# Performance work log

Measured on AMD Instinct MI355X. Metric: run time of the kernel, lower is better.

## Reference

```python
import jax, jax.numpy as jnp
import numpy as np

D = 1024
B, N = 4, 2048

def setup_inputs() -> dict:
    key = jax.random.key(0)
    ks = jax.random.split(key, 7)
    sc = 1.0 / np.sqrt(D)
    return {
        "x": jax.random.normal(ks[0], (B, N, D), dtype=jnp.float32),
        "wq_w": jax.random.normal(ks[1], (D, D), dtype=jnp.float32) * sc,
        "wq_b": jax.random.normal(ks[2], (D,), dtype=jnp.float32) * 0.01,
        "wk_w": jax.random.normal(ks[3], (D, D), dtype=jnp.float32) * sc,
        "wk_b": jax.random.normal(ks[4], (D,), dtype=jnp.float32) * 0.01,
        "wv_w": jax.random.normal(ks[5], (D, D), dtype=jnp.float32) * sc,
        "wv_b": jax.random.normal(ks[6], (D,), dtype=jnp.float32) * 0.01,
    }

def reference(x, wq_w, wq_b, wk_w, wk_b, wv_w, wv_b):
    # torch Linear: y = x @ W^T + b
    q = x @ wq_w.T + wq_b
    k = x @ wk_w.T + wk_b
    v = x @ wv_w.T + wv_b
    d = q.shape[-1]
    s = jnp.einsum("bid,bjd->bij", q, k) / jnp.sqrt(jnp.float32(d))
    # faithful to original: triu then transpose (zeros, NOT -inf, enter the softmax)
    t = jnp.swapaxes(jnp.triu(s), -2, -1)
    p = jax.nn.softmax(t, axis=-2)
    attn = jnp.swapaxes(jnp.triu(p), -2, -1) @ v
    return attn
```

## Files before the change

kernel.cpp:

```cpp
#include <hip/hip_runtime.h>
#include <hip/hip_fp16.h>
#include <cstdint>

typedef _Float16 half8_t __attribute__((ext_vector_type(8)));
typedef float f32x4 __attribute__((ext_vector_type(4)));

#define D_ 1024
#define B_ 4
#define N_ 2048
#define M_ (B_*N_)
#define NC_ 3072

#define OFF_WCAT  0u
#define OFF_BCAT  6291456u
#define OFF_XB    6303744u
#define OFF_Q     23080960u
#define OFF_K     39858176u
#define OFF_V     56635392u
#define OFF_ZP    73412608u
#define OFF_DEXP  74461184u
#define OFF_SV    74493952u
#define OFF_INVD  74756096u
#define OFF_CD    74788864u

__device__ __forceinline__ void gload_lds16(const void* g, void* l) {
  __builtin_amdgcn_global_load_lds(
      (const __attribute__((address_space(1))) unsigned int*)(uintptr_t)g,
      (__attribute__((address_space(3))) unsigned int*)(uintptr_t)l, 16, 0, 0);
}

__device__ __forceinline__ void stage128x64(const __half* rowbase, char* lds, int tid) {
#pragma unroll
  for (int inst = 0; inst < 4; ++inst) {
    int L  = inst * 4096 + tid * 16;
    int r  = L >> 7;
    int cb = L & 127;
    int cbs = cb ^ ((r & 7) << 4);
    gload_lds16((const char*)rowbase + (size_t)r * (D_ * 2) + cbs, lds + L);
  }
}

__device__ __forceinline__ half8_t ldsfrag(const char* lds, int row, int cbyte) {
  int b = (row << 7) + (cbyte ^ ((row & 7) << 4));
  return *reinterpret_cast<const half8_t*>(lds + b);
}

__device__ __forceinline__ void gemm128_core(const __half* Arow0, const __half* Brow0,
                                             char* As, char* Bs, f32x4 acc[4][4]) {
  const int tid  = threadIdx.x;
  const int lane = tid & 63;
  const int wave = tid >> 6;
  const int wm = wave >> 1, wn = wave & 1;
  for (int kt = 0; kt < 16; ++kt) {
    if (kt) __syncthreads();
    stage128x64(Arow0 + kt * 64, As, tid);
    stage128x64(Brow0 + kt * 64, Bs, tid);
    asm volatile("s_waitcnt vmcnt(0)" ::: "memory");
    __syncthreads();
#pragma unroll
    for (int kk = 0; kk < 2; ++kk) {
      const int cbyte = kk * 64 + (lane >> 4) * 16;
      half8_t a[4], b[4];
#pragma unroll
      for (int mf = 0; mf < 4; ++mf) a[mf] = ldsfrag(As, wm * 64 + mf * 16 + (lane & 15), cbyte);
#pragma unroll
      for (int nf = 0; nf < 4; ++nf) b[nf] = ldsfrag(Bs, wn * 64 + nf * 16 + (lane & 15), cbyte);
#pragma unroll
      for (int mf = 0; mf < 4; ++mf)
#pragma unroll
        for (int nf = 0; nf < 4; ++nf)
          acc[mf][nf] = __builtin_amdgcn_mfma_f32_16x16x32_f16(a[mf], b[nf], acc[mf][nf], 0, 0, 0);
    }
  }
}

__global__ __launch_bounds__(256) void k_prep(
    const float* __restrict__ x, const float* __restrict__ wq, const float* __restrict__ wk,
    const float* __restrict__ wv, const float* __restrict__ bq, const float* __restrict__ bk,
    const float* __restrict__ bv, __half* __restrict__ xb, __half* __restrict__ wcat,
    float* __restrict__ bcat, float* __restrict__ Zpart) {
  const int NX4 = (M_ * D_) / 4;
  const int NW4 = (D_ * D_) / 4;
  const int TOT = NX4 + 3 * NW4;
  int tid0 = blockIdx.x * 256 + threadIdx.x;
  int stride = gridDim.x * 256;
  for (int i = tid0; i < TOT; i += stride) {
    float4 f; __half* dst;
    if (i < NX4) {
      f = ((const float4*)x)[i];
      dst = xb + 4 * (size_t)i;
    } else {
      int j = i - NX4; int w = j / NW4; int o = j - w * NW4;
      const float* src = (w == 0) ? wq : (w == 1) ? wk : wv;
      f = ((const float4*)src)[o];
      dst = wcat + (size_t)w * (D_ * D_) + 4 * (size_t)o;
    }
    __half h0 = __float2half(f.x), h1 = __float2half(f.y),
           h2 = __float2half(f.z), h3 = __float2half(f.w);
    ushort4 u = { __half_as_ushort(h0), __half_as_ushort(h1),
                  __half_as_ushort(h2), __half_as_ushort(h3) };
    *((ushort4*)dst) = u;
  }
  if (tid0 < NC_)
    bcat[tid0] = (tid0 < 1024) ? bq[tid0] : (tid0 < 2048) ? bk[tid0 - 1024] : bv[tid0 - 2048];
  for (int i = tid0; i < M_ * 32; i += stride) Zpart[i] = 0.f;
}

__global__ __launch_bounds__(256) void k_qkv(
    const __half* __restrict__ xb, const __half* __restrict__ wcat,
    const float* __restrict__ bcat,
    __half* __restrict__ q, __half* __restrict__ kx, __half* __restrict__ v) {
  __shared__ __align__(16) char smem[32768];
  char* As = smem; char* Bs = smem + 16384;
  int bid = blockIdx.x;
  int bm = bid / 24, bn = bid % 24;
  f32x4 acc[4][4];
#pragma unroll
  for (int i = 0; i < 4; ++i)
#pragma unroll
    for (int j = 0; j < 4; ++j) acc[i][j] = f32x4{0.f, 0.f, 0.f, 0.f};
  gemm128_core(xb + (size_t)bm * 128 * D_, wcat + (size_t)bn * 128 * D_, As, Bs, acc);

  const int lane = threadIdx.x & 63;
  const int wave = threadIdx.x >> 6;
  const int wm = wave >> 1, wn = wave & 1;
  int sel = bn >> 3;
  __half* outp = (sel == 0) ? q : (sel == 1) ? kx : v;
#pragma unroll
  for (int nf = 0; nf < 4; ++nf) {
    int nloc = wn * 64 + nf * 16 + (lane & 15);
    float bias = bcat[bn * 128 + nloc];
    int ncol = (bn & 7) * 128 + nloc;
#pragma unroll
    for (int mf = 0; mf < 4; ++mf) {
#pragma unroll
      for (int r = 0; r < 4; ++r) {
        int m = bm * 128 + wm * 64 + mf * 16 + (lane >> 4) * 4 + r;
        outp[(size_t)m * D_ + ncol] = __float2half(acc[mf][nf][r] + bias);
      }
    }
  }
}

__global__ __launch_bounds__(256) void k_stats(
    const __half* __restrict__ q, const __half* __restrict__ kx,
    float* __restrict__ Zpart, float* __restrict__ dexp) {
  __shared__ __align__(16) char smem[32768];
  int bid = blockIdx.x;
  int b = bid / 136;
  int r = bid % 136;
  int ti = 0;
  while (r >= 16 - ti) { r -= 16 - ti; ++ti; }
  int tj = ti + r;

  f32x4 acc[4][4];
#pragma unroll
  for (int i = 0; i < 4; ++i)
#pragma unroll
    for (int j = 0; j < 4; ++j) acc[i][j] = f32x4{0.f, 0.f, 0.f, 0.f};
  const size_t base = (size_t)b * N_ * D_;
  gemm128_core(q + base + (size_t)ti * 128 * D_, kx + base + (size_t)tj * 128 * D_,
               smem, smem + 16384, acc);

  const int lane = threadIdx.x & 63;
  const int wave = threadIdx.x >> 6;
  const int wm = wave >> 1, wn = wave & 1;
  const bool offd = (tj > ti);
  const float scale = 0.03125f;
  int zrow0 = b * N_ + ti * 128;
#pragma unroll
  for (int mf = 0; mf < 4; ++mf) {
#pragma unroll
    for (int rg = 0; rg < 4; ++rg) {
      int il = wm * 64 + mf * 16 + (lane >> 4) * 4 + rg;
      float ssum = 0.f;
#pragma unroll
      for (int nf = 0; nf < 4; ++nf) {
        int jl = wn * 64 + nf * 16 + (lane & 15);
        float e = __expf(acc[mf][nf][rg] * scale);
        bool keep = offd || (jl >= il);
        if (!offd && jl == il) dexp[zrow0 + il] = e;
        ssum += keep ? e : 0.f;
      }
      ssum += __shfl_xor(ssum, 1);
      ssum += __shfl_xor(ssum, 2);
      ssum += __shfl_xor(ssum, 4);
      ssum += __shfl_xor(ssum, 8);
      if ((lane & 15) == 0)
        Zpart[(size_t)(zrow0 + il) * 32 + tj * 2 + wn] = ssum;
    }
  }
}

__global__ __launch_bounds__(256) void k_mid(
    const __half* __restrict__ v, const float* __restrict__ Zpart,
    const float* __restrict__ dexp, float* __restrict__ Sv,
    float* __restrict__ invD, float* __restrict__ cdiag) {
  int tid = blockIdx.x * 256 + threadIdx.x;
  int b = tid >> 14, c = (tid >> 10) & 15, d = tid & 1023;
  const __half* vp = v + ((size_t)(b * N_ + c * 128)) * D_ + d;
  float s = 0.f;
#pragma unroll 8
  for (int r2 = 0; r2 < 128; ++r2) s += __half2float(vp[(size_t)r2 * D_]);
  Sv[tid] = s;
  if (tid < M_) {
    float z = 0.f;
#pragma unroll
    for (int t = 0; t < 32; ++t) z += Zpart[(size_t)tid * 32 + t];
    float Dd = (float)(tid & (N_ - 1)) + z;
    float iv = 1.f / Dd;
    invD[tid] = iv;
    cdiag[tid] = dexp[tid] * iv;
  }
}

__global__ __launch_bounds__(256) void k_out(
    const __half* __restrict__ v, const float* __restrict__ Sv,
    const float* __restrict__ invD, const float* __restrict__ cdiag,
    float* __restrict__ out) {
  int tid = blockIdx.x * 256 + threadIdx.x;
  int b = tid >> 14, c = (tid >> 10) & 15, d = tid & 1023;
  float run = 0.f;
  for (int cc = 0; cc < c; ++cc) run += Sv[((b << 4) + cc) * 1024 + d];
  const __half* vp = v + ((size_t)(b * N_ + c * 128)) * D_ + d;
  float* op = out + ((size_t)(b * N_ + c * 128)) * D_ + d;
  int zi0 = b * N_ + c * 128;
#pragma unroll 4
  for (int r2 = 0; r2 < 128; ++r2) {
    float vi = __half2float(vp[(size_t)r2 * D_]);
    op[(size_t)r2 * D_] = run * invD[zi0 + r2] + cdiag[zi0 + r2] * vi;
    run += vi;
  }
}

extern "C" void kernel_launch(void* const* d_in, const int* in_sizes, int n_in,
                              void* d_out, int out_size, void* d_ws, size_t ws_size,
                              hipStream_t stream) {
  const float* x  = (const float*)d_in[0];
  const float* wq = (const float*)d_in[1];
  const float* bq = (const float*)d_in[2];
  const float* wk = (const float*)d_in[3];
  const float* bk = (const float*)d_in[4];
  const float* wv = (const float*)d_in[5];
  const float* bv = (const float*)d_in[6];
  float* out = (float*)d_out;
  char* ws = (char*)d_ws;

  __half* wcat = (__half*)(ws + OFF_WCAT);
  float*  bcat = (float*)(ws + OFF_BCAT);
  __half* xb   = (__half*)(ws + OFF_XB);
  __half* q    = (__half*)(ws + OFF_Q);
  __half* k    = (__half*)(ws + OFF_K);
  __half* v    = (__half*)(ws + OFF_V);
  float* Zpart = (float*)(ws + OFF_ZP);
  float* dexp  = (float*)(ws + OFF_DEXP);
  float* Sv    = (float*)(ws + OFF_SV);
  float* invD  = (float*)(ws + OFF_INVD);
  float* cdiag = (float*)(ws + OFF_CD);

  k_prep<<<dim3(2048), dim3(256), 0, stream>>>(x, wq, wk, wv, bq, bk, bv, xb, wcat, bcat, Zpart);
  k_qkv<<<dim3(64 * 24), dim3(256), 0, stream>>>(xb, wcat, bcat, q, k, v);
  k_stats<<<dim3(4 * 136), dim3(256), 0, stream>>>(q, k, Zpart, dexp);
  k_mid<<<dim3(256), dim3(256), 0, stream>>>(v, Zpart, dexp, Sv, invD, cdiag);
  k_out<<<dim3(256), dim3(256), 0, stream>>>(v, Sv, invD, cdiag, out);
}
```

Baseline: 141.7 us.

## Replace 128x128 GEMM core with double-buffered 256x256 phased MFMA pipeline

```diff
diff --git a/kernel.cpp b/kernel.cpp
--- a/kernel.cpp
+++ b/kernel.cpp
@@ -29,48 +29,116 @@
       (__attribute__((address_space(3))) unsigned int*)(uintptr_t)l, 16, 0, 0);
 }
 
-__device__ __forceinline__ void stage128x64(const __half* rowbase, char* lds, int tid) {
-#pragma unroll
-  for (int inst = 0; inst < 4; ++inst) {
-    int L  = inst * 4096 + tid * 16;
-    int r  = L >> 7;
-    int cb = L & 127;
-    int cbs = cb ^ ((r & 7) << 4);
-    gload_lds16((const char*)rowbase + (size_t)r * (D_ * 2) + cbs, lds + L);
-  }
-}
-
-__device__ __forceinline__ half8_t ldsfrag(const char* lds, int row, int cbyte) {
-  int b = (row << 7) + (cbyte ^ ((row & 7) << 4));
-  return *reinterpret_cast<const half8_t*>(lds + b);
-}
-
-__device__ __forceinline__ void gemm128_core(const __half* Arow0, const __half* Brow0,
-                                             char* As, char* Bs, f32x4 acc[4][4]) {
+
+__device__ __forceinline__ void calc_soff(int tid, int soff[4]) {
+#pragma unroll
+  for (int i = 0; i < 4; ++i) {
+    int L = i * 8192 + tid * 16;
+    int s = L >> 10;
+    int w = L & 1023;
+    w ^= ((w >> 9) & 1) << 5;
+    int r  = (s >> 1) * 16 + (w >> 6);
+    int kb = (s & 1) * 64 + (w & 63);
+    soff[i] = r * 2048 + kb;
+  }
+}
+
+#define MFMA_QUAD(QM, QN)                                                     \
+  _Pragma("unroll")                                                           \
+  for (int ks = 0; ks < 2; ++ks)                                              \
+    _Pragma("unroll")                                                         \
+    for (int mf = 0; mf < 4; ++mf)                                            \
+      _Pragma("unroll")                                                       \
+      for (int nf = 0; nf < 2; ++nf)                                          \
+        acc[(QM)*4 + mf][(QN)*2 + nf] = __builtin_amdgcn_mfma_f32_16x16x32_f16( \
+            a[mf][ks], b[(QN)][nf][ks], acc[(QM)*4 + mf][(QN)*2 + nf], 0, 0, 0);
+
+__device__ __forceinline__ void gemm256_8ph(const char* Ag, const char* Bg,
+                                            char* smem, f32x4 acc[8][4]) {
   const int tid  = threadIdx.x;
   const int lane = tid & 63;
   const int wave = tid >> 6;
-  const int wm = wave >> 1, wn = wave & 1;
-  for (int kt = 0; kt < 16; ++kt) {
-    if (kt) __syncthreads();
-    stage128x64(Arow0 + kt * 64, As, tid);
-    stage128x64(Brow0 + kt * 64, Bs, tid);
-    asm volatile("s_waitcnt vmcnt(0)" ::: "memory");
-    __syncthreads();
-#pragma unroll
-    for (int kk = 0; kk < 2; ++kk) {
-      const int cbyte = kk * 64 + (lane >> 4) * 16;
-      half8_t a[4], b[4];
-#pragma unroll
-      for (int mf = 0; mf < 4; ++mf) a[mf] = ldsfrag(As, wm * 64 + mf * 16 + (lane & 15), cbyte);
-#pragma unroll
-      for (int nf = 0; nf < 4; ++nf) b[nf] = ldsfrag(Bs, wn * 64 + nf * 16 + (lane & 15), cbyte);
-#pragma unroll
-      for (int mf = 0; mf < 4; ++mf)
-#pragma unroll
-        for (int nf = 0; nf < 4; ++nf)
-          acc[mf][nf] = __builtin_amdgcn_mfma_f32_16x16x32_f16(a[mf], b[nf], acc[mf][nf], 0, 0, 0);
-    }
+  const int wm = wave >> 2, wn = wave & 3;
+
+  int soff[4];
+  calc_soff(tid, soff);
+  const int wlane = (((lane & 15) * 64 + (lane >> 4) * 16)) ^ (((lane >> 3) & 1) << 5);
+
+#pragma unroll
+  for (int i = 0; i < 4; ++i) gload_lds16(Ag + soff[i], smem + i * 8192 + tid * 16);
+#pragma unroll
+  for (int i = 0; i < 4; ++i) gload_lds16(Bg + soff[i], smem + 32768 + i * 8192 + tid * 16);
+  asm volatile("s_waitcnt vmcnt(0)" ::: "memory");
+  __builtin_amdgcn_s_barrier();
+
+  for (int t = 0; t < 16; ++t) {
+    char* A0  = smem + ((t & 1) << 16);
+    char* B0  = A0 + 32768;
+    char* A1  = smem + (((t + 1) & 1) << 16);
+    char* B1s = A1 + 32768;
+    const half8_t* ap = (const half8_t*)(A0 + wm * 16384 + wlane);
+    const half8_t* bp = (const half8_t*)(B0 + wn * 8192 + wlane);
+    const char* Agn = Ag + (t + 1) * 128;
+    const char* Bgn = Bg + (t + 1) * 128;
+    const bool pre = (t < 15);
+
+    half8_t a[4][2];
+    half8_t b[2][2][2];
+
+#pragma unroll
+    for (int mf = 0; mf < 4; ++mf)
+#pragma unroll
+      for (int ks = 0; ks < 2; ++ks)
+        a[mf][ks] = ap[(mf * 2 + ks) * 64];
+#pragma unroll
+    for (int nf = 0; nf < 2; ++nf)
+#pragma unroll
+      for (int ks = 0; ks < 2; ++ks)
+        b[0][nf][ks] = bp[(nf * 2 + ks) * 64];
+    if (pre) {
+#pragma unroll
+      for (int i = 0; i < 4; ++i) gload_lds16(Agn + soff[i], A1 + i * 8192 + tid * 16);
+    }
+    __builtin_amdgcn_s_barrier();
+    asm volatile("s_waitcnt lgkmcnt(0)" ::: "memory");
+    __builtin_amdgcn_s_setprio(1);
+    MFMA_QUAD(0, 0)
+    __builtin_amdgcn_s_setprio(0);
+    __builtin_amdgcn_s_barrier();
+
+#pragma unroll
+    for (int nf = 0; nf < 2; ++nf)
+#pragma unroll
+      for (int ks = 0; ks < 2; ++ks)
+        b[1][nf][ks] = bp[((2 + nf) * 2 + ks) * 64];
+    if (pre) {
+#pragma unroll
+      for (int i = 0; i < 4; ++i) gload_lds16(Bgn + soff[i], B1s + i * 8192 + tid * 16);
+    }
+    __builtin_amdgcn_s_barrier();
+    asm volatile("s_waitcnt lgkmcnt(0)" ::: "memory");
+    __builtin_amdgcn_s_setprio(1);
+    MFMA_QUAD(0, 1)
+    __builtin_amdgcn_s_setprio(0);
+    __builtin_amdgcn_s_barrier();
+
+#pragma unroll
+    for (int mf = 0; mf < 4; ++mf)
+#pragma unroll
+      for (int ks = 0; ks < 2; ++ks)
+        a[mf][ks] = ap[((4 + mf) * 2 + ks) * 64];
+    __builtin_amdgcn_s_barrier();
+    asm volatile("s_waitcnt lgkmcnt(0)" ::: "memory");
+    __builtin_amdgcn_s_setprio(1);
+    MFMA_QUAD(1, 0)
+    __builtin_amdgcn_s_setprio(0);
+    __builtin_amdgcn_s_barrier();
+
+    __builtin_amdgcn_s_setprio(1);
+    MFMA_QUAD(1, 1)
+    __builtin_amdgcn_s_setprio(0);
+    if (pre) asm volatile("s_waitcnt vmcnt(0)" ::: "memory");
+    __builtin_amdgcn_s_barrier();
   }
 }
 
@@ -106,80 +174,85 @@
   for (int i = tid0; i < M_ * 32; i += stride) Zpart[i] = 0.f;
 }
 
-__global__ __launch_bounds__(256) void k_qkv(
+__global__ __launch_bounds__(512, 2) void k_qkv256(
     const __half* __restrict__ xb, const __half* __restrict__ wcat,
     const float* __restrict__ bcat,
     __half* __restrict__ q, __half* __restrict__ kx, __half* __restrict__ v) {
-  __shared__ __align__(16) char smem[32768];
-  char* As = smem; char* Bs = smem + 16384;
+  __shared__ __align__(16) char smem[131072];
   int bid = blockIdx.x;
-  int bm = bid / 24, bn = bid % 24;
-  f32x4 acc[4][4];
-#pragma unroll
-  for (int i = 0; i < 4; ++i)
+  int tile = (bid & 7) * 48 + (bid >> 3);
+  int bm = tile / 12, bn = tile % 12;
+
+  f32x4 acc[8][4];
+#pragma unroll
+  for (int i = 0; i < 8; ++i)
 #pragma unroll
     for (int j = 0; j < 4; ++j) acc[i][j] = f32x4{0.f, 0.f, 0.f, 0.f};
-  gemm128_core(xb + (size_t)bm * 128 * D_, wcat + (size_t)bn * 128 * D_, As, Bs, acc);
+
+  gemm256_8ph((const char*)(xb + (size_t)bm * 256 * D_),
+              (const char*)(wcat + (size_t)bn * 256 * D_), smem, acc);
 
   const int lane = threadIdx.x & 63;
   const int wave = threadIdx.x >> 6;
-  const int wm = wave >> 1, wn = wave & 1;
-  int sel = bn >> 3;
+  const int wm = wave >> 2, wn = wave & 3;
+  int sel = bn >> 2;
   __half* outp = (sel == 0) ? q : (sel == 1) ? kx : v;
+  int colbase = (bn & 3) * 256 + wn * 64;
 #pragma unroll
   for (int nf = 0; nf < 4; ++nf) {
-    int nloc = wn * 64 + nf * 16 + (lane & 15);
-    float bias = bcat[bn * 128 + nloc];
-    int ncol = (bn & 7) * 128 + nloc;
-#pragma unroll
-    for (int mf = 0; mf < 4; ++mf) {
-#pragma unroll
-      for (int r = 0; r < 4; ++r) {
-        int m = bm * 128 + wm * 64 + mf * 16 + (lane >> 4) * 4 + r;
-        outp[(size_t)m * D_ + ncol] = __float2half(acc[mf][nf][r] + bias);
+    int nloc = colbase + nf * 16 + (lane & 15);
+    float bias = bcat[bn * 256 + wn * 64 + nf * 16 + (lane & 15)];
+#pragma unroll
+    for (int mf = 0; mf < 8; ++mf) {
+#pragma unroll
+      for (int rr = 0; rr < 4; ++rr) {
+        int m = bm * 256 + wm * 128 + mf * 16 + (lane >> 4) * 4 + rr;
+        outp[(size_t)m * D_ + nloc] = __float2half(acc[mf][nf][rr] + bias);
       }
     }
   }
 }
 
-__global__ __launch_bounds__(256) void k_stats(
+__global__ __launch_bounds__(512, 2) void k_stats256(
     const __half* __restrict__ q, const __half* __restrict__ kx,
     float* __restrict__ Zpart, float* __restrict__ dexp) {
-  __shared__ __align__(16) char smem[32768];
+  __shared__ __align__(16) char smem[131072];
   int bid = blockIdx.x;
-  int b = bid / 136;
-  int r = bid % 136;
+  int tile = (bid & 7) * 18 + (bid >> 3);
+  int b = tile / 36;
+  int r = tile % 36;
   int ti = 0;
-  while (r >= 16 - ti) { r -= 16 - ti; ++ti; }
+  while (r >= 8 - ti) { r -= 8 - ti; ++ti; }
   int tj = ti + r;
 
-  f32x4 acc[4][4];
-#pragma unroll
-  for (int i = 0; i < 4; ++i)
+  f32x4 acc[8][4];
+#pragma unroll
+  for (int i = 0; i < 8; ++i)
 #pragma unroll
     for (int j = 0; j < 4; ++j) acc[i][j] = f32x4{0.f, 0.f, 0.f, 0.f};
+
   const size_t base = (size_t)b * N_ * D_;
-  gemm128_core(q + base + (size_t)ti * 128 * D_, kx + base + (size_t)tj * 128 * D_,
-               smem, smem + 16384, acc);
+  gemm256_8ph((const char*)(q + base + (size_t)ti * 256 * D_),
+              (const char*)(kx + base + (size_t)tj * 256 * D_), smem, acc);
 
   const int lane = threadIdx.x & 63;
   const int wave = threadIdx.x >> 6;
-  const int wm = wave >> 1, wn = wave & 1;
+  const int wm = wave >> 2, wn = wave & 3;
   const bool offd = (tj > ti);
   const float scale = 0.03125f;
-  int zrow0 = b * N_ + ti * 128;
-#pragma unroll
-  for (int mf = 0; mf < 4; ++mf) {
-#pragma unroll
-    for (int rg = 0; rg < 4; ++rg) {
-      int il = wm * 64 + mf * 16 + (lane >> 4) * 4 + rg;
+  int zr0 = b * N_ + ti * 256;
+#pragma unroll
+  for (int mf = 0; mf < 8; ++mf) {
+#pragma unroll
+    for (int rr = 0; rr < 4; ++rr) {
+      int il = wm * 128 + mf * 16 + (lane >> 4) * 4 + rr;
       float ssum = 0.f;
 #pragma unroll
       for (int nf = 0; nf < 4; ++nf) {
         int jl = wn * 64 + nf * 16 + (lane & 15);
-        float e = __expf(acc[mf][nf][rg] * scale);
+        float e = __expf(acc[mf][nf][rr] * scale);
         bool keep = offd || (jl >= il);
-        if (!offd && jl == il) dexp[zrow0 + il] = e;
+        if (!offd && jl == il) dexp[zr0 + il] = e;
         ssum += keep ? e : 0.f;
       }
       ssum += __shfl_xor(ssum, 1);
@@ -187,7 +260,7 @@
       ssum += __shfl_xor(ssum, 4);
       ssum += __shfl_xor(ssum, 8);
       if ((lane & 15) == 0)
-        Zpart[(size_t)(zrow0 + il) * 32 + tj * 2 + wn] = ssum;
+        Zpart[(size_t)(zr0 + il) * 32 + tj * 4 + wn] = ssum;
     }
   }
 }
@@ -259,8 +332,8 @@
   float* cdiag = (float*)(ws + OFF_CD);
 
   k_prep<<<dim3(2048), dim3(256), 0, stream>>>(x, wq, wk, wv, bq, bk, bv, xb, wcat, bcat, Zpart);
-  k_qkv<<<dim3(64 * 24), dim3(256), 0, stream>>>(xb, wcat, bcat, q, k, v);
-  k_stats<<<dim3(4 * 136), dim3(256), 0, stream>>>(q, k, Zpart, dexp);
+  k_qkv256<<<dim3(384), dim3(512), 0, stream>>>(xb, wcat, bcat, q, k, v);
+  k_stats256<<<dim3(144), dim3(512), 0, stream>>>(q, k, Zpart, dexp);
   k_mid<<<dim3(256), dim3(256), 0, stream>>>(v, Zpart, dexp, Sv, invD, cdiag);
   k_out<<<dim3(256), dim3(256), 0, stream>>>(v, Sv, invD, cdiag, out);
 }
```

New measurement: 142.3 us. Within noise of the previous version (+0.5%).

## Replace QKV projection GEMM with 256x192 tile, double-buffered LDS pipeline

Applied to the files above, without the earlier changes.

```diff
diff --git a/kernel.cpp b/kernel.cpp
--- a/kernel.cpp
+++ b/kernel.cpp
@@ -73,6 +73,65 @@
     }
   }
 }
+
+
+#define G01(QM)                                                              \
+  _Pragma("unroll") for (int ks = 0; ks < 2; ++ks)                           \
+  _Pragma("unroll") for (int mf = 0; mf < 4; ++mf)                           \
+  _Pragma("unroll") for (int nf = 0; nf < 2; ++nf)                           \
+    acc[(QM)*4+mf][nf] = __builtin_amdgcn_mfma_f32_16x16x32_f16(             \
+        a[mf][ks], b[nf][ks], acc[(QM)*4+mf][nf], 0, 0, 0);
+
+#define G2(QM)                                                               \
+  _Pragma("unroll") for (int ks = 0; ks < 2; ++ks)                           \
+  _Pragma("unroll") for (int mf = 0; mf < 4; ++mf)                           \
+    acc[(QM)*4+mf][2] = __builtin_amdgcn_mfma_f32_16x16x32_f16(              \
+        a[mf][ks], b[2][ks], acc[(QM)*4+mf][2], 0, 0, 0);
+
+#define QKV_HALF(APTR, BPTR, AgN, BgN, PRE)                                  \
+  {                                                                          \
+    const half8_t* ap = (const half8_t*)((APTR) + wm * 16384 + wlane);       \
+    const half8_t* bp = (const half8_t*)((BPTR) + wn * 6144  + wlane);       \
+                                \
+    _Pragma("unroll") for (int mf = 0; mf < 4; ++mf)                         \
+    _Pragma("unroll") for (int ks = 0; ks < 2; ++ks)                         \
+      a[mf][ks] = ap[(mf * 2 + ks) * 64];                                    \
+    _Pragma("unroll") for (int nf = 0; nf < 2; ++nf)                         \
+    _Pragma("unroll") for (int ks = 0; ks < 2; ++ks)                         \
+      b[nf][ks] = bp[(nf * 2 + ks) * 64];                                    \
+    __builtin_amdgcn_s_barrier();                                            \
+    asm volatile("s_waitcnt lgkmcnt(0)" ::: "memory");                       \
+    __builtin_amdgcn_s_setprio(1); G01(0) __builtin_amdgcn_s_setprio(0);     \
+    __builtin_amdgcn_s_barrier();                                            \
+                                            \
+    _Pragma("unroll") for (int ks = 0; ks < 2; ++ks)                         \
+      b[2][ks] = bp[(4 + ks) * 64];                                          \
+    __builtin_amdgcn_s_barrier();                                            \
+    asm volatile("s_waitcnt lgkmcnt(0)" ::: "memory");                       \
+    __builtin_amdgcn_s_setprio(1); G2(0) __builtin_amdgcn_s_setprio(0);      \
+    __builtin_amdgcn_s_barrier();                                            \
+                                           \
+    _Pragma("unroll") for (int mf = 0; mf < 4; ++mf)                         \
+    _Pragma("unroll") for (int ks = 0; ks < 2; ++ks)                         \
+      a[mf][ks] = ap[((4 + mf) * 2 + ks) * 64];                              \
+    __builtin_amdgcn_s_barrier();                                            \
+    asm volatile("s_waitcnt lgkmcnt(0)" ::: "memory");                       \
+    __builtin_amdgcn_s_setprio(1); G01(1) __builtin_amdgcn_s_setprio(0);     \
+    __builtin_amdgcn_s_barrier();                                            \
+             \
+    if (PRE) {                                                               \
+      _Pragma("unroll") for (int i2 = 0; i2 < 4; ++i2)                       \
+        gload_lds16((AgN) + soffA[i2], (APTR) + i2 * 8192 + tid * 16);       \
+      _Pragma("unroll") for (int i2 = 0; i2 < 3; ++i2)                       \
+        gload_lds16((BgN) + soffB[i2], (BPTR) + i2 * 8192 + tid * 16);       \
+    }                                                                        \
+    __builtin_amdgcn_s_barrier();                                            \
+    asm volatile("s_waitcnt lgkmcnt(0)" ::: "memory");                       \
+    __builtin_amdgcn_s_setprio(1); G2(1) __builtin_amdgcn_s_setprio(0);      \
+    if (PRE) asm volatile("s_waitcnt vmcnt(7)" ::: "memory");                \
+    else     asm volatile("s_waitcnt vmcnt(0)" ::: "memory");                \
+    __builtin_amdgcn_s_barrier();                                            \
+  }
 
 __global__ __launch_bounds__(256) void k_prep(
     const float* __restrict__ x, const float* __restrict__ wq, const float* __restrict__ wk,
@@ -106,37 +165,87 @@
   for (int i = tid0; i < M_ * 32; i += stride) Zpart[i] = 0.f;
 }
 
-__global__ __launch_bounds__(256) void k_qkv(
+__global__ __launch_bounds__(512, 2) void k_qkv192(
     const __half* __restrict__ xb, const __half* __restrict__ wcat,
     const float* __restrict__ bcat,
     __half* __restrict__ q, __half* __restrict__ kx, __half* __restrict__ v) {
-  __shared__ __align__(16) char smem[32768];
-  char* As = smem; char* Bs = smem + 16384;
+  __shared__ __align__(16) char smem[114688];
+  const int tid  = threadIdx.x;
+  const int lane = tid & 63;
+  const int wave = tid >> 6;
+  const int wm = wave >> 2, wn = wave & 3;
+
   int bid = blockIdx.x;
-  int bm = bid / 24, bn = bid % 24;
-  f32x4 acc[4][4];
-#pragma unroll
-  for (int i = 0; i < 4; ++i)
-#pragma unroll
-    for (int j = 0; j < 4; ++j) acc[i][j] = f32x4{0.f, 0.f, 0.f, 0.f};
-  gemm128_core(xb + (size_t)bm * 128 * D_, wcat + (size_t)bn * 128 * D_, As, Bs, acc);
-
-  const int lane = threadIdx.x & 63;
-  const int wave = threadIdx.x >> 6;
-  const int wm = wave >> 1, wn = wave & 1;
-  int sel = bn >> 3;
-  __half* outp = (sel == 0) ? q : (sel == 1) ? kx : v;
-#pragma unroll
-  for (int nf = 0; nf < 4; ++nf) {
-    int nloc = wn * 64 + nf * 16 + (lane & 15);
-    float bias = bcat[bn * 128 + nloc];
-    int ncol = (bn & 7) * 128 + nloc;
-#pragma unroll
-    for (int mf = 0; mf < 4; ++mf) {
-#pragma unroll
-      for (int r = 0; r < 4; ++r) {
-        int m = bm * 128 + wm * 64 + mf * 16 + (lane >> 4) * 4 + r;
-        outp[(size_t)m * D_ + ncol] = __float2half(acc[mf][nf][r] + bias);
+  int tile = (bid & 7) * 64 + (bid >> 3);
+  int bm = tile >> 4, bn = tile & 15;
+
+  float bias[3];
+#pragma unroll
+  for (int nf = 0; nf < 3; ++nf)
+    bias[nf] = bcat[bn * 192 + wn * 48 + nf * 16 + (lane & 15)];
+  asm volatile("" :: "v"(bias[0]), "v"(bias[1]), "v"(bias[2]));
+
+  int soffA[4], soffB[3];
+#pragma unroll
+  for (int i = 0; i < 4; ++i) {
+    int L = i * 8192 + tid * 16;
+    int s = L >> 10, w = L & 1023;
+    w ^= ((w >> 9) & 1) << 5;
+    soffA[i] = ((s >> 1) * 16 + (w >> 6)) * 2048 + ((s & 1) * 64 + (w & 63));
+  }
+#pragma unroll
+  for (int i = 0; i < 3; ++i) {
+    int L = i * 8192 + tid * 16;
+    int s = L >> 10, w = L & 1023;
+    w ^= ((w >> 9) & 1) << 5;
+    soffB[i] = ((s >> 1) * 16 + (w >> 6)) * 2048 + ((s & 1) * 64 + (w & 63));
+  }
+  const int wlane = (((lane & 15) * 64 + (lane >> 4) * 16)) ^ (((lane >> 3) & 1) << 5);
+
+  const char* Ag = (const char*)(xb + (size_t)bm * 256 * D_);
+  const char* Bg = (const char*)(wcat + (size_t)bn * 192 * D_);
+  char* A0 = smem;           char* B0 = smem + 32768;
+  char* A1 = smem + 57344;   char* B1 = smem + 90112;
+
+  f32x4 acc[8][3];
+#pragma unroll
+  for (int i = 0; i < 8; ++i)
+#pragma unroll
+    for (int j = 0; j < 3; ++j) acc[i][j] = f32x4{0.f, 0.f, 0.f, 0.f};
+
+#pragma unroll
+  for (int i = 0; i < 4; ++i) gload_lds16(Ag + soffA[i], A0 + i * 8192 + tid * 16);
+#pragma unroll
+  for (int i = 0; i < 3; ++i) gload_lds16(Bg + soffB[i], B0 + i * 8192 + tid * 16);
+#pragma unroll
+  for (int i = 0; i < 4; ++i) gload_lds16(Ag + 128 + soffA[i], A1 + i * 8192 + tid * 16);
+#pragma unroll
+  for (int i = 0; i < 3; ++i) gload_lds16(Bg + 128 + soffB[i], B1 + i * 8192 + tid * 16);
+  asm volatile("s_waitcnt vmcnt(7)" ::: "memory");
+  __builtin_amdgcn_s_barrier();
+
+  half8_t a[4][2], b[3][2];
+  for (int it = 0; it < 8; ++it) {
+    const bool pre = (it < 7);
+    const char* Ag2 = Ag + (2 * it + 2) * 128;
+    const char* Bg2 = Bg + (2 * it + 2) * 128;
+    const char* Ag3 = Ag + (2 * it + 3) * 128;
+    const char* Bg3 = Bg + (2 * it + 3) * 128;
+    QKV_HALF(A0, B0, Ag2, Bg2, pre)
+    QKV_HALF(A1, B1, Ag3, Bg3, pre)
+  }
+
+#pragma unroll
+  for (int nf = 0; nf < 3; ++nf) {
+    int gcol = bn * 192 + wn * 48 + nf * 16 + (lane & 15);
+    int sel = gcol >> 10, col = gcol & 1023;
+    __half* outp = (sel == 0) ? q : (sel == 1) ? kx : v;
+#pragma unroll
+    for (int mf = 0; mf < 8; ++mf) {
+#pragma unroll
+      for (int rr = 0; rr < 4; ++rr) {
+        int m = bm * 256 + wm * 128 + mf * 16 + (lane >> 4) * 4 + rr;
+        outp[(size_t)m * D_ + col] = __float2half(acc[mf][nf][rr] + bias[nf]);
       }
     }
   }
@@ -259,7 +368,7 @@
   float* cdiag = (float*)(ws + OFF_CD);
 
   k_prep<<<dim3(2048), dim3(256), 0, stream>>>(x, wq, wk, wv, bq, bk, bv, xb, wcat, bcat, Zpart);
-  k_qkv<<<dim3(64 * 24), dim3(256), 0, stream>>>(xb, wcat, bcat, q, k, v);
+  k_qkv192<<<dim3(512), dim3(512), 0, stream>>>(xb, wcat, bcat, q, k, v);
   k_stats<<<dim3(4 * 136), dim3(256), 0, stream>>>(q, k, Zpart, dexp);
   k_mid<<<dim3(256), dim3(256), 0, stream>>>(v, Zpart, dexp, Sv, invD, cdiag);
   k_out<<<dim3(256), dim3(256), 0, stream>>>(v, Sv, invD, cdiag, out);
```

After: 144.5 us. 2.0% more time.

## Fuse all stages into one persistent kernel with hierarchical grid barriers

Applied to the files above, without the earlier changes.

```diff
diff --git a/kernel.cpp b/kernel.cpp
--- a/kernel.cpp
+++ b/kernel.cpp
@@ -10,6 +10,7 @@
 #define N_ 2048
 #define M_ (B_*N_)
 #define NC_ 3072
+#define NBLK 768
 
 #define OFF_WCAT  0u
 #define OFF_BCAT  6291456u
@@ -20,8 +21,7 @@
 #define OFF_ZP    73412608u
 #define OFF_DEXP  74461184u
 #define OFF_SV    74493952u
-#define OFF_INVD  74756096u
-#define OFF_CD    74788864u
+#define OFF_BAR   75542528u
 
 __device__ __forceinline__ void gload_lds16(const void* g, void* l) {
   __builtin_amdgcn_global_load_lds(
@@ -74,162 +74,216 @@
   }
 }
 
-__global__ __launch_bounds__(256) void k_prep(
-    const float* __restrict__ x, const float* __restrict__ wq, const float* __restrict__ wk,
-    const float* __restrict__ wv, const float* __restrict__ bq, const float* __restrict__ bk,
-    const float* __restrict__ bv, __half* __restrict__ xb, __half* __restrict__ wcat,
-    float* __restrict__ bcat, float* __restrict__ Zpart) {
-  const int NX4 = (M_ * D_) / 4;
-  const int NW4 = (D_ * D_) / 4;
-  const int TOT = NX4 + 3 * NW4;
-  int tid0 = blockIdx.x * 256 + threadIdx.x;
-  int stride = gridDim.x * 256;
-  for (int i = tid0; i < TOT; i += stride) {
-    float4 f; __half* dst;
-    if (i < NX4) {
-      f = ((const float4*)x)[i];
-      dst = xb + 4 * (size_t)i;
+__device__ __forceinline__ int bar_ld(int* p) {
+  return __hip_atomic_load(p, __ATOMIC_ACQUIRE, __HIP_MEMORY_SCOPE_AGENT);
+}
+
+__device__ __forceinline__ void gridbar(int* bar, int phase) {
+  __syncthreads();
+  if (threadIdx.x == 0) {
+    __threadfence();
+    int g = blockIdx.x >> 5;
+    int* grp_cnt = bar + 32 + g * 16;
+    int* grp_gen = bar + 416 + g * 16;
+    if (atomicAdd(grp_cnt, 1) == 31) {
+      if (atomicAdd(bar + 0, 1) == 23) {
+        atomicExch(bar + 0, 0);
+        __threadfence();
+        atomicAdd(bar + 16, 1);
+      } else {
+        while (bar_ld(bar + 16) <= phase) __builtin_amdgcn_s_sleep(2);
+      }
+      atomicExch(grp_cnt, 0);
+      __threadfence();
+      atomicAdd(grp_gen, 1);
     } else {
-      int j = i - NX4; int w = j / NW4; int o = j - w * NW4;
-      const float* src = (w == 0) ? wq : (w == 1) ? wk : wv;
-      f = ((const float4*)src)[o];
-      dst = wcat + (size_t)w * (D_ * D_) + 4 * (size_t)o;
-    }
-    __half h0 = __float2half(f.x), h1 = __float2half(f.y),
-           h2 = __float2half(f.z), h3 = __float2half(f.w);
-    ushort4 u = { __half_as_ushort(h0), __half_as_ushort(h1),
-                  __half_as_ushort(h2), __half_as_ushort(h3) };
-    *((ushort4*)dst) = u;
-  }
-  if (tid0 < NC_)
-    bcat[tid0] = (tid0 < 1024) ? bq[tid0] : (tid0 < 2048) ? bk[tid0 - 1024] : bv[tid0 - 2048];
-  for (int i = tid0; i < M_ * 32; i += stride) Zpart[i] = 0.f;
-}
-
-__global__ __launch_bounds__(256) void k_qkv(
-    const __half* __restrict__ xb, const __half* __restrict__ wcat,
-    const float* __restrict__ bcat,
-    __half* __restrict__ q, __half* __restrict__ kx, __half* __restrict__ v) {
+      while (bar_ld(grp_gen) <= phase) __builtin_amdgcn_s_sleep(2);
+    }
+    __threadfence();
+  }
+  __syncthreads();
+}
+
+__global__ __launch_bounds__(256, 3) void k_mega(
+    const float* __restrict__ x, const float* __restrict__ wq, const float* __restrict__ bq,
+    const float* __restrict__ wk, const float* __restrict__ bk,
+    const float* __restrict__ wv, const float* __restrict__ bv,
+    __half* __restrict__ xb, __half* __restrict__ wcat, float* __restrict__ bcat,
+    __half* __restrict__ q, __half* __restrict__ kx, __half* __restrict__ v,
+    float* __restrict__ Zpart, float* __restrict__ dexp, float* __restrict__ Sv,
+    float* __restrict__ out, int* bar) {
   __shared__ __align__(16) char smem[32768];
-  char* As = smem; char* Bs = smem + 16384;
-  int bid = blockIdx.x;
-  int bm = bid / 24, bn = bid % 24;
-  f32x4 acc[4][4];
-#pragma unroll
-  for (int i = 0; i < 4; ++i)
-#pragma unroll
-    for (int j = 0; j < 4; ++j) acc[i][j] = f32x4{0.f, 0.f, 0.f, 0.f};
-  gemm128_core(xb + (size_t)bm * 128 * D_, wcat + (size_t)bn * 128 * D_, As, Bs, acc);
-
-  const int lane = threadIdx.x & 63;
-  const int wave = threadIdx.x >> 6;
-  const int wm = wave >> 1, wn = wave & 1;
-  int sel = bn >> 3;
-  __half* outp = (sel == 0) ? q : (sel == 1) ? kx : v;
-#pragma unroll
-  for (int nf = 0; nf < 4; ++nf) {
-    int nloc = wn * 64 + nf * 16 + (lane & 15);
-    float bias = bcat[bn * 128 + nloc];
-    int ncol = (bn & 7) * 128 + nloc;
+  __shared__ float sInv[32], sCd[32];
+  const int bid = blockIdx.x;
+  const int thr = threadIdx.x;
+  const int lane = thr & 63;
+  const int wave = thr >> 6;
+
+  {
+    const int NX4 = (M_ * D_) / 4;
+    const int NW4 = (D_ * D_) / 4;
+    const int TOT = NX4 + 3 * NW4;
+    int tid0 = bid * 256 + thr;
+    const int stride = NBLK * 256;
+    for (int i = tid0; i < TOT; i += stride) {
+      float4 f; __half* dst;
+      if (i < NX4) {
+        f = ((const float4*)x)[i];
+        dst = xb + 4 * (size_t)i;
+      } else {
+        int j = i - NX4; int w = j / NW4; int o = j - w * NW4;
+        const float* src = (w == 0) ? wq : (w == 1) ? wk : wv;
+        f = ((const float4*)src)[o];
+        dst = wcat + (size_t)w * (D_ * D_) + 4 * (size_t)o;
+      }
+      ushort4 u = { __half_as_ushort(__float2half(f.x)), __half_as_ushort(__float2half(f.y)),
+                    __half_as_ushort(__float2half(f.z)), __half_as_ushort(__float2half(f.w)) };
+      *((ushort4*)dst) = u;
+    }
+    if (tid0 < NC_)
+      bcat[tid0] = (tid0 < 1024) ? bq[tid0] : (tid0 < 2048) ? bk[tid0 - 1024] : bv[tid0 - 2048];
+  }
+  gridbar(bar, 0);
+
+  {
+    const int wm = wave >> 1, wn = wave & 1;
+#pragma unroll 1
+    for (int t = bid; t < 1536; t += NBLK) {
+      int bm = t / 24, bn = t % 24;
+      f32x4 acc[4][4];
+#pragma unroll
+      for (int i = 0; i < 4; ++i)
+#pragma unroll
+        for (int j = 0; j < 4; ++j) acc[i][j] = f32x4{0.f, 0.f, 0.f, 0.f};
+      gemm128_core(xb + (size_t)bm * 128 * D_, wcat + (size_t)bn * 128 * D_,
+                   smem, smem + 16384, acc);
+      int sel = bn >> 3;
+      __half* outp = (sel == 0) ? q : (sel == 1) ? kx : v;
+#pragma unroll
+      for (int nf = 0; nf < 4; ++nf) {
+        int nloc = wn * 64 + nf * 16 + (lane & 15);
+        float bias = bcat[bn * 128 + nloc];
+        int ncol = (bn & 7) * 128 + nloc;
+#pragma unroll
+        for (int mf = 0; mf < 4; ++mf) {
+#pragma unroll
+          for (int r = 0; r < 4; ++r) {
+            int m = bm * 128 + wm * 64 + mf * 16 + (lane >> 4) * 4 + r;
+            outp[(size_t)m * D_ + ncol] = __float2half(acc[mf][nf][r] + bias);
+          }
+        }
+      }
+      __syncthreads();
+    }
+  }
+  gridbar(bar, 1);
+
+  if (bid < 544) {
+    int b = bid / 136;
+    int r = bid % 136;
+    int ti = 0;
+    while (r >= 16 - ti) { r -= 16 - ti; ++ti; }
+    int tj = ti + r;
+
+    f32x4 acc[4][4];
+#pragma unroll
+    for (int i = 0; i < 4; ++i)
+#pragma unroll
+      for (int j = 0; j < 4; ++j) acc[i][j] = f32x4{0.f, 0.f, 0.f, 0.f};
+    const size_t base = (size_t)b * N_ * D_;
+    gemm128_core(q + base + (size_t)ti * 128 * D_, kx + base + (size_t)tj * 128 * D_,
+                 smem, smem + 16384, acc);
+
+    const int wm = wave >> 1, wn = wave & 1;
+    const bool offd = (tj > ti);
+    const float scale = 0.03125f;
+    int zrow0 = b * N_ + ti * 128;
 #pragma unroll
     for (int mf = 0; mf < 4; ++mf) {
 #pragma unroll
-      for (int r = 0; r < 4; ++r) {
-        int m = bm * 128 + wm * 64 + mf * 16 + (lane >> 4) * 4 + r;
-        outp[(size_t)m * D_ + ncol] = __float2half(acc[mf][nf][r] + bias);
-      }
-    }
-  }
-}
-
-__global__ __launch_bounds__(256) void k_stats(
-    const __half* __restrict__ q, const __half* __restrict__ kx,
-    float* __restrict__ Zpart, float* __restrict__ dexp) {
-  __shared__ __align__(16) char smem[32768];
-  int bid = blockIdx.x;
-  int b = bid / 136;
-  int r = bid % 136;
-  int ti = 0;
-  while (r >= 16 - ti) { r -= 16 - ti; ++ti; }
-  int tj = ti + r;
-
-  f32x4 acc[4][4];
-#pragma unroll
-  for (int i = 0; i < 4; ++i)
-#pragma unroll
-    for (int j = 0; j < 4; ++j) acc[i][j] = f32x4{0.f, 0.f, 0.f, 0.f};
-  const size_t base = (size_t)b * N_ * D_;
-  gemm128_core(q + base + (size_t)ti * 128 * D_, kx + base + (size_t)tj * 128 * D_,
-               smem, smem + 16384, acc);
-
-  const int lane = threadIdx.x & 63;
-  const int wave = threadIdx.x >> 6;
-  const int wm = wave >> 1, wn = wave & 1;
-  const bool offd = (tj > ti);
-  const float scale = 0.03125f;
-  int zrow0 = b * N_ + ti * 128;
-#pragma unroll
-  for (int mf = 0; mf < 4; ++mf) {
-#pragma unroll
-    for (int rg = 0; rg < 4; ++rg) {
-      int il = wm * 64 + mf * 16 + (lane >> 4) * 4 + rg;
-      float ssum = 0.f;
-#pragma unroll
-      for (int nf = 0; nf < 4; ++nf) {
-        int jl = wn * 64 + nf * 16 + (lane & 15);
-        float e = __expf(acc[mf][nf][rg] * scale);
-        bool keep = offd || (jl >= il);
-        if (!offd && jl == il) dexp[zrow0 + il] = e;
-        ssum += keep ? e : 0.f;
-      }
-      ssum += __shfl_xor(ssum, 1);
-      ssum += __shfl_xor(ssum, 2);
-      ssum += __shfl_xor(ssum, 4);
-      ssum += __shfl_xor(ssum, 8);
-      if ((lane & 15) == 0)
-        Zpart[(size_t)(zrow0 + il) * 32 + tj * 2 + wn] = ssum;
-    }
-  }
-}
-
-__global__ __launch_bounds__(256) void k_mid(
-    const __half* __restrict__ v, const float* __restrict__ Zpart,
-    const float* __restrict__ dexp, float* __restrict__ Sv,
-    float* __restrict__ invD, float* __restrict__ cdiag) {
-  int tid = blockIdx.x * 256 + threadIdx.x;
-  int b = tid >> 14, c = (tid >> 10) & 15, d = tid & 1023;
-  const __half* vp = v + ((size_t)(b * N_ + c * 128)) * D_ + d;
-  float s = 0.f;
+      for (int rg = 0; rg < 4; ++rg) {
+        int il = wm * 64 + mf * 16 + (lane >> 4) * 4 + rg;
+        float ssum = 0.f;
+#pragma unroll
+        for (int nf = 0; nf < 4; ++nf) {
+          int jl = wn * 64 + nf * 16 + (lane & 15);
+          float e = __expf(acc[mf][nf][rg] * scale);
+          bool keep = offd || (jl >= il);
+          if (!offd && jl == il) dexp[zrow0 + il] = e;
+          ssum += keep ? e : 0.f;
+        }
+        ssum += __shfl_xor(ssum, 1);
+        ssum += __shfl_xor(ssum, 2);
+        ssum += __shfl_xor(ssum, 4);
+        ssum += __shfl_xor(ssum, 8);
+        if ((lane & 15) == 0)
+          Zpart[(size_t)(zrow0 + il) * 32 + tj * 2 + wn] = ssum;
+      }
+    }
+  } else {
+    int s0 = bid - 544;
+#pragma unroll 1
+    for (int rep = 0; rep < 2; ++rep) {
+      int slab = (rep == 0) ? s0 : 224 + s0;
+      if (rep == 1 && s0 >= 32) break;
+      int b = slab >> 6, c = slab & 63;
+      int d0 = thr * 4;
+      const ushort4* vp = (const ushort4*)(v + ((size_t)(b * N_ + c * 32)) * D_ + d0);
+      f32x4 s = {0.f, 0.f, 0.f, 0.f};
 #pragma unroll 8
-  for (int r2 = 0; r2 < 128; ++r2) s += __half2float(vp[(size_t)r2 * D_]);
-  Sv[tid] = s;
-  if (tid < M_) {
-    float z = 0.f;
-#pragma unroll
-    for (int t = 0; t < 32; ++t) z += Zpart[(size_t)tid * 32 + t];
-    float Dd = (float)(tid & (N_ - 1)) + z;
-    float iv = 1.f / Dd;
-    invD[tid] = iv;
-    cdiag[tid] = dexp[tid] * iv;
-  }
-}
-
-__global__ __launch_bounds__(256) void k_out(
-    const __half* __restrict__ v, const float* __restrict__ Sv,
-    const float* __restrict__ invD, const float* __restrict__ cdiag,
-    float* __restrict__ out) {
-  int tid = blockIdx.x * 256 + threadIdx.x;
-  int b = tid >> 14, c = (tid >> 10) & 15, d = tid & 1023;
-  float run = 0.f;
-  for (int cc = 0; cc < c; ++cc) run += Sv[((b << 4) + cc) * 1024 + d];
-  const __half* vp = v + ((size_t)(b * N_ + c * 128)) * D_ + d;
-  float* op = out + ((size_t)(b * N_ + c * 128)) * D_ + d;
-  int zi0 = b * N_ + c * 128;
+      for (int r2 = 0; r2 < 32; ++r2) {
+        ushort4 u = vp[r2 * (D_ / 4)];
+        s[0] += __half2float(__ushort_as_half(u.x));
+        s[1] += __half2float(__ushort_as_half(u.y));
+        s[2] += __half2float(__ushort_as_half(u.z));
+        s[3] += __half2float(__ushort_as_half(u.w));
+      }
+      *(f32x4*)(Sv + (size_t)slab * D_ + d0) = s;
+    }
+  }
+  gridbar(bar, 2);
+
+  if (bid < 256) {
+    int b = bid >> 6, c = bid & 63;
+    int d0 = thr * 4;
+    int zi0 = b * N_ + c * 32;
+
+    if (thr < 32) {
+      int i  = c * 32 + thr;
+      int row = zi0 + thr;
+      int t0 = (i >> 7) * 2;
+      float z = 0.f;
+      for (int t = t0; t < 32; ++t) z += Zpart[(size_t)row * 32 + t];
+      float iv = 1.f / ((float)i + z);
+      sInv[thr] = iv;
+      sCd[thr]  = dexp[row] * iv;
+    }
+    __syncthreads();
+
+    f32x4 run = {0.f, 0.f, 0.f, 0.f};
+    for (int cc = 0; cc < c; ++cc) {
+      f32x4 sv = *(const f32x4*)(Sv + (size_t)((b << 6) + cc) * D_ + d0);
+      run[0] += sv[0]; run[1] += sv[1]; run[2] += sv[2]; run[3] += sv[3];
+    }
+    const ushort4* vp = (const ushort4*)(v + (size_t)zi0 * D_ + d0);
+    float* op = out + (size_t)zi0 * D_ + d0;
 #pragma unroll 4
-  for (int r2 = 0; r2 < 128; ++r2) {
-    float vi = __half2float(vp[(size_t)r2 * D_]);
-    op[(size_t)r2 * D_] = run * invD[zi0 + r2] + cdiag[zi0 + r2] * vi;
-    run += vi;
+    for (int r2 = 0; r2 < 32; ++r2) {
+      ushort4 u = vp[r2 * (D_ / 4)];
+      f32x4 vi;
+      vi[0] = __half2float(__ushort_as_half(u.x));
+      vi[1] = __half2float(__ushort_as_half(u.y));
+      vi[2] = __half2float(__ushort_as_half(u.z));
+      vi[3] = __half2float(__ushort_as_half(u.w));
+      float iv = sInv[r2], cd = sCd[r2];
+      f32x4 o;
+      o[0] = run[0] * iv + cd * vi[0];
+      o[1] = run[1] * iv + cd * vi[1];
+      o[2] = run[2] * iv + cd * vi[2];
+      o[3] = run[3] * iv + cd * vi[3];
+      *(f32x4*)(op + (size_t)r2 * D_) = o;
+      run[0] += vi[0]; run[1] += vi[1]; run[2] += vi[2]; run[3] += vi[3];
+    }
   }
 }
 
@@ -255,12 +309,9 @@
   float* Zpart = (float*)(ws + OFF_ZP);
   float* dexp  = (float*)(ws + OFF_DEXP);
   float* Sv    = (float*)(ws + OFF_SV);
-  float* invD  = (float*)(ws + OFF_INVD);
-  float* cdiag = (float*)(ws + OFF_CD);
-
-  k_prep<<<dim3(2048), dim3(256), 0, stream>>>(x, wq, wk, wv, bq, bk, bv, xb, wcat, bcat, Zpart);
-  k_qkv<<<dim3(64 * 24), dim3(256), 0, stream>>>(xb, wcat, bcat, q, k, v);
-  k_stats<<<dim3(4 * 136), dim3(256), 0, stream>>>(q, k, Zpart, dexp);
-  k_mid<<<dim3(256), dim3(256), 0, stream>>>(v, Zpart, dexp, Sv, invD, cdiag);
-  k_out<<<dim3(256), dim3(256), 0, stream>>>(v, Sv, invD, cdiag, out);
-}
+  int*   bar   = (int*)(ws + OFF_BAR);
+
+  hipMemsetAsync((void*)bar, 0, 4096, stream);
+  k_mega<<<dim3(NBLK), dim3(256), 0, stream>>>(
+      x, wq, bq, wk, bk, wv, bv, xb, wcat, bcat, q, k, v, Zpart, dexp, Sv, out, bar);
+}
```

Measured after the change: 522.4 us. 3.69x slower.
